# Kernel optimization log

Measured on AMD Instinct MI355X. Metric: run time of the kernel, lower is better.

Reference implementation:

```python
import jax, jax.numpy as jnp
import numpy as np

N = 50000   # nodes
E = 800000  # edges (avg degree 16)
H = 8       # num_heads
D = 16      # head_dim = hidden_size // num_heads = 128 // 8


def setup_inputs() -> dict:
    key = jax.random.key(0)
    k1, k2, k3, k4, k5 = jax.random.split(key, 5)
    q = jax.random.normal(k1, (N, D, H), dtype=jnp.float32)
    k = jax.random.normal(k2, (N, D, H), dtype=jnp.float32)
    v = jax.random.normal(k3, (N, D, H), dtype=jnp.float32)
    # COO adjacency: row = destination node of each edge, col = source node
    row = jnp.sort(jax.random.randint(k4, (E,), 0, N, dtype=jnp.int32))
    col = jax.random.randint(k5, (E,), 0, N, dtype=jnp.int32)
    return {"q": q, "k": k, "v": v, "row": row, "col": col}


def reference(q, k, v, row, col):
    # bsddmm: sampled dense-dense matmul -> per-edge, per-head attention logits
    # logits[e, h] = sum_d q[row[e], d, h] * k[col[e], d, h]
    logits = jnp.einsum('edh,edh->eh', q[row], k[col])  # [E, H]

    # sparse softmax over each destination row (per head), numerically stable
    m = jax.ops.segment_max(logits, row, num_segments=N)  # [N, H]
    p = jnp.exp(logits - m[row])                          # [E, H]
    s = jax.ops.segment_sum(p, row, num_segments=N)       # [N, H]
    attn = p / s[row]                                     # [E, H]

    # bspmm: out[i, d, h] = sum_{e: row[e]==i} attn[e, h] * v[col[e], d, h]
    out = jax.ops.segment_sum(attn[:, None, :] * v[col], row, num_segments=N)  # [N, D, H]
    return out.reshape(N, -1)  # [N, D*H]
```

## Files before the change

### kernel.cpp

```cpp
#include <hip/hip_runtime.h>
#include <math.h>

#define HEADS 8
#define DIM 16
#define NODES_PER_BLOCK 32

__global__ __launch_bounds__(256) void spmha_kernel(
    const float* __restrict__ q, const float* __restrict__ k, const float* __restrict__ v,
    const int* __restrict__ row, const int* __restrict__ col,
    float* __restrict__ out, int N, int E) {
  __shared__ int rp[NODES_PER_BLOCK + 1];

  int node0 = blockIdx.x * NODES_PER_BLOCK;

  if (threadIdx.x <= NODES_PER_BLOCK) {
    int target = node0 + threadIdx.x;
    int lo = 0, hi = E;
    while (lo < hi) {
      int mid = (lo + hi) >> 1;
      if (row[mid] < target) lo = mid + 1; else hi = mid;
    }
    rp[threadIdx.x] = lo;
  }
  __syncthreads();

  int t = blockIdx.x * blockDim.x + threadIdx.x;
  if (t >= N * HEADS) return;
  int il = threadIdx.x >> 3;
  int i  = node0 + il;
  int h  = threadIdx.x & 7;

  int s = rp[il];
  int e = rp[il + 1];

  const float* qb = q + (size_t)i * 128 + h;
  float qv[DIM];
#pragma unroll
  for (int d = 0; d < DIM; ++d) qv[d] = qb[d * 8];

  float m = -INFINITY;
  float den = 0.f;
  float o[DIM];
#pragma unroll
  for (int d = 0; d < DIM; ++d) o[d] = 0.f;

  for (int eidx = s; eidx < e; ++eidx) {
    int c = col[eidx];
    const float* kb = k + (size_t)c * 128 + h;
    const float* vb = v + (size_t)c * 128 + h;

    float l = 0.f;
#pragma unroll
    for (int d = 0; d < DIM; ++d) l = fmaf(qv[d], kb[d * 8], l);

    float mn = fmaxf(m, l);
    float scale = __expf(m - mn);
    float p = __expf(l - mn);
    den = fmaf(den, scale, p);
#pragma unroll
    for (int d = 0; d < DIM; ++d) o[d] = fmaf(o[d], scale, p * vb[d * 8]);
    m = mn;
  }

  float inv = (e > s) ? 1.f / den : 0.f;
  float* ob = out + (size_t)i * 128 + h;
#pragma unroll
  for (int d = 0; d < DIM; ++d) ob[d * 8] = o[d] * inv;
}

extern "C" void kernel_launch(void* const* d_in, const int* in_sizes, int n_in,
                              void* d_out, int out_size, void* d_ws, size_t ws_size,
                              hipStream_t stream) {
  const float* q   = (const float*)d_in[0];
  const float* k   = (const float*)d_in[1];
  const float* v   = (const float*)d_in[2];
  const int*   row = (const int*)d_in[3];
  const int*   col = (const int*)d_in[4];
  float* out = (float*)d_out;

  int N = in_sizes[0] / (DIM * HEADS);
  int E = in_sizes[3];

  int total = N * HEADS;
  int grid = (total + 255) / 256;
  spmha_kernel<<<grid, 256, 0, stream>>>(q, k, v, row, col, out, N, E);
}
```

Before: 228.7 us.

## Vectorize per-node loads with float4 lanes and shuffle-reduce head dot products

Each group of 8 threads now loads a node's 128-float q/k/v row as float4 chunks instead of strided scalar loads. Each lane holds 4 heads times 4 d-slices, so the dot products are finished with xor shuffles across lanes. Every lane keeps online-softmax state for 4 heads. Edges are processed two at a time so more loads are in flight. This is meant to cut the number of memory instructions and improve coalescing of the gathered rows, at the cost of extra shuffles, duplicated exp work per lane, and higher register pressure.

After: 231.5 us. About the same (+1.2%).

```diff
diff --git a/kernel.cpp b/kernel.cpp
--- a/kernel.cpp
+++ b/kernel.cpp
@@ -3,17 +3,17 @@
 
 #define HEADS 8
 #define DIM 16
-#define NODES_PER_BLOCK 32
+#define NPB 32
 
 __global__ __launch_bounds__(256) void spmha_kernel(
     const float* __restrict__ q, const float* __restrict__ k, const float* __restrict__ v,
     const int* __restrict__ row, const int* __restrict__ col,
     float* __restrict__ out, int N, int E) {
-  __shared__ int rp[NODES_PER_BLOCK + 1];
+  __shared__ int rp[NPB + 1];
 
-  int node0 = blockIdx.x * NODES_PER_BLOCK;
+  int node0 = blockIdx.x * NPB;
 
-  if (threadIdx.x <= NODES_PER_BLOCK) {
+  if (threadIdx.x <= NPB) {
     int target = node0 + threadIdx.x;
     int lo = 0, hi = E;
     while (lo < hi) {
@@ -24,48 +24,102 @@
   }
   __syncthreads();
 
-  int t = blockIdx.x * blockDim.x + threadIdx.x;
-  if (t >= N * HEADS) return;
   int il = threadIdx.x >> 3;
   int i  = node0 + il;
-  int h  = threadIdx.x & 7;
+  int l  = threadIdx.x & 7;
+  bool alive = (i < N);
 
-  int s = rp[il];
-  int e = rp[il + 1];
+  int s = alive ? rp[il] : 0;
+  int e = alive ? rp[il + 1] : 0;
 
-  const float* qb = q + (size_t)i * 128 + h;
-  float qv[DIM];
+  float qv[16];
+  if (alive) {
+    const float4* qb = (const float4*)(q + (size_t)i * 128);
 #pragma unroll
-  for (int d = 0; d < DIM; ++d) qv[d] = qb[d * 8];
-
-  float m = -INFINITY;
-  float den = 0.f;
-  float o[DIM];
-#pragma unroll
-  for (int d = 0; d < DIM; ++d) o[d] = 0.f;
-
-  for (int eidx = s; eidx < e; ++eidx) {
-    int c = col[eidx];
-    const float* kb = k + (size_t)c * 128 + h;
-    const float* vb = v + (size_t)c * 128 + h;
-
-    float l = 0.f;
-#pragma unroll
-    for (int d = 0; d < DIM; ++d) l = fmaf(qv[d], kb[d * 8], l);
-
-    float mn = fmaxf(m, l);
-    float scale = __expf(m - mn);
-    float p = __expf(l - mn);
-    den = fmaf(den, scale, p);
-#pragma unroll
-    for (int d = 0; d < DIM; ++d) o[d] = fmaf(o[d], scale, p * vb[d * 8]);
-    m = mn;
+    for (int r = 0; r < 4; ++r) *(float4*)&qv[4 * r] = qb[8 * r + l];
   }
 
-  float inv = (e > s) ? 1.f / den : 0.f;
-  float* ob = out + (size_t)i * 128 + h;
+  float o[16];
 #pragma unroll
-  for (int d = 0; d < DIM; ++d) ob[d * 8] = o[d] * inv;
+  for (int x = 0; x < 16; ++x) o[x] = 0.f;
+  float m[4], den[4];
+#pragma unroll
+  for (int j = 0; j < 4; ++j) { m[j] = -INFINITY; den[j] = 0.f; }
+
+  auto do_edge = [&](const float* kk, const float* vv) {
+    float part[4];
+#pragma unroll
+    for (int j = 0; j < 4; ++j) part[j] = 0.f;
+#pragma unroll
+    for (int r = 0; r < 4; ++r)
+#pragma unroll
+      for (int j = 0; j < 4; ++j)
+        part[j] = fmaf(qv[4 * r + j], kk[4 * r + j], part[j]);
+#pragma unroll
+    for (int j = 0; j < 4; ++j) {
+      part[j] += __shfl_xor(part[j], 2);
+      part[j] += __shfl_xor(part[j], 4);
+    }
+#pragma unroll
+    for (int j = 0; j < 4; ++j) {
+      float mn = fmaxf(m[j], part[j]);
+      float sc = __expf(m[j] - mn);
+      float p  = __expf(part[j] - mn);
+      den[j] = fmaf(den[j], sc, p);
+      m[j] = mn;
+#pragma unroll
+      for (int r = 0; r < 4; ++r)
+        o[4 * r + j] = fmaf(o[4 * r + j], sc, p * vv[4 * r + j]);
+    }
+  };
+
+  int eidx = s;
+  for (; eidx + 2 <= e; eidx += 2) {
+    int c0 = col[eidx];
+    int c1 = col[eidx + 1];
+    const float4* kb0 = (const float4*)(k + (size_t)c0 * 128);
+    const float4* vb0 = (const float4*)(v + (size_t)c0 * 128);
+    const float4* kb1 = (const float4*)(k + (size_t)c1 * 128);
+    const float4* vb1 = (const float4*)(v + (size_t)c1 * 128);
+    float kk0[16], vv0[16], kk1[16], vv1[16];
+#pragma unroll
+    for (int r = 0; r < 4; ++r) {
+      *(float4*)&kk0[4 * r] = kb0[8 * r + l];
+      *(float4*)&vv0[4 * r] = vb0[8 * r + l];
+      *(float4*)&kk1[4 * r] = kb1[8 * r + l];
+      *(float4*)&vv1[4 * r] = vb1[8 * r + l];
+    }
+    do_edge(kk0, vv0);
+    do_edge(kk1, vv1);
+  }
+  if (eidx < e) {
+    int c0 = col[eidx];
+    const float4* kb0 = (const float4*)(k + (size_t)c0 * 128);
+    const float4* vb0 = (const float4*)(v + (size_t)c0 * 128);
+    float kk0[16], vv0[16];
+#pragma unroll
+    for (int r = 0; r < 4; ++r) {
+      *(float4*)&kk0[4 * r] = kb0[8 * r + l];
+      *(float4*)&vv0[4 * r] = vb0[8 * r + l];
+    }
+    do_edge(kk0, vv0);
+  }
+
+  if (alive) {
+    float inv[4];
+#pragma unroll
+    for (int j = 0; j < 4; ++j) inv[j] = (e > s) ? 1.f / den[j] : 0.f;
+    float4* ob = (float4*)(out + (size_t)i * 128);
+#pragma unroll
+    for (int r = 0; r < 4; ++r) {
+      float4 res;
+      res.x = o[4 * r + 0] * inv[0];
+      res.y = o[4 * r + 1] * inv[1];
+      res.z = o[4 * r + 2] * inv[2];
+      res.w = o[4 * r + 3] * inv[3];
+      ob[8 * r + l] = res;
+    }
+  }
 }
 
 extern "C" void kernel_launch(void* const* d_in, const int* in_sizes, int n_in,
```
